# Performance work log

Measured on AMD Instinct MI355X. Metric: run time of the kernel, lower is better.

The kernel has to match this reference:

```python
import jax, jax.numpy as jnp
import numpy as np

N_NODES = 50000
LN_EPS = 1e-5


def gcn_conv(x, src, dst, norm, W, b):
    # PyG GCNConv: h = x @ W, then symmetric-normalized scatter-add, then bias.
    h = x @ W                                   # [N, out]
    msg = h[src] * norm[:, None]                # [E+N, out] gathered, scaled
    out = jax.ops.segment_sum(msg, dst, num_segments=N_NODES)
    return out + b


def layer_norm(x, gamma, beta):
    mu = jnp.mean(x, axis=-1, keepdims=True)
    var = jnp.var(x, axis=-1, keepdims=True)
    return (x - mu) * jax.lax.rsqrt(var + LN_EPS) * gamma + beta


def setup_inputs() -> dict:
    key = jax.random.key(0)
    ks = jax.random.split(key, 8)
    N, E, D = N_NODES, 1600000, 128
    x = jax.random.normal(ks[0], (N, D), dtype=jnp.float32)
    edge_index = jax.random.randint(ks[1], (2, E), 0, N, dtype=jnp.int64)
    s = 1.0 / np.sqrt(D)
    return {
        "x": x,
        "edge_index": edge_index,
        "W1": jax.random.uniform(ks[2], (D, D), jnp.float32, -s, s),
        "b1": jnp.zeros((D,), jnp.float32),
        "g1": jnp.ones((D,), jnp.float32),
        "be1": jnp.zeros((D,), jnp.float32),
        "W2": jax.random.uniform(ks[3], (D, D), jnp.float32, -s, s),
        "b2": jnp.zeros((D,), jnp.float32),
        "g2": jnp.ones((D,), jnp.float32),
        "be2": jnp.zeros((D,), jnp.float32),
    }


def reference(x, edge_index, W1, b1, g1, be1, W2, b2, g2, be2):
    # Add self-loops (PyG GCNConv default add_self_loops=True)
    sl = jnp.arange(N_NODES, dtype=edge_index.dtype)
    src = jnp.concatenate([edge_index[0], sl])
    dst = jnp.concatenate([edge_index[1], sl])
    # Symmetric normalization: deg^{-1/2}[src] * deg^{-1/2}[dst]
    deg = jax.ops.segment_sum(jnp.ones_like(src, dtype=x.dtype), dst,
                              num_segments=N_NODES)
    dinv = jnp.where(deg > 0, jax.lax.rsqrt(deg), 0.0)
    norm = dinv[src] * dinv[dst]

    h = gcn_conv(x, src, dst, norm, W1, b1)
    h = jax.nn.elu(layer_norm(h, g1, be1))
    h = gcn_conv(h, src, dst, norm, W2, b2)
    h = jax.nn.elu(layer_norm(h, g2, be2))
    return h
```

## Files before the change

### kernel.cpp

```cpp
#include <hip/hip_runtime.h>
#include <hip/hip_bf16.h>
#include <math.h>

#define N_NODES 50000
#define D 128
#define LN_EPS 1e-5f
#define NB 391
#define CHUNK 4096
#define GB 782
#define HB 512

typedef unsigned int u32;
typedef unsigned short u16;
typedef __attribute__((ext_vector_type(8))) short bf16x8;
typedef __attribute__((ext_vector_type(4))) float f32x4;

static __device__ __forceinline__ u16 f2bf(float f) {
    union { float f; unsigned u; } v; v.f = f;
    unsigned r = v.u + 0x7fff + ((v.u >> 16) & 1);
    return (u16)(r >> 16);
}
static __device__ __forceinline__ float bf2f(u16 b) {
    union { unsigned u; float f; } v; v.u = ((unsigned)b) << 16;
    return v.f;
}

static __device__ __forceinline__ bf16x8 packf8(const float* p) {
    float4 f0 = *(const float4*)p;
    float4 f1 = *(const float4*)(p + 4);
    bf16x8 r;
    r[0] = (short)f2bf(f0.x); r[1] = (short)f2bf(f0.y);
    r[2] = (short)f2bf(f0.z); r[3] = (short)f2bf(f0.w);
    r[4] = (short)f2bf(f1.x); r[5] = (short)f2bf(f1.y);
    r[6] = (short)f2bf(f1.z); r[7] = (short)f2bf(f1.w);
    return r;
}

__global__ __launch_bounds__(256) void gemm1_hist(const float* __restrict__ X,
                                                  const float* __restrict__ W,
                                                  u16* __restrict__ H,
                                                  const int* __restrict__ dstA,
                                                  u32* __restrict__ bucketCount, int E) {
    __shared__ __align__(16) u16 WT[D][136];
    __shared__ u32 hist[NB];

    if (blockIdx.x >= GB) {
        for (int b = threadIdx.x; b < NB; b += 256) hist[b] = 0;
        __syncthreads();
        int stride = HB * 256;
        for (int e = (blockIdx.x - GB) * 256 + threadIdx.x; e < E; e += stride)
            atomicAdd(&hist[((u32)dstA[e]) >> 7], 1u);
        __syncthreads();
        for (int b = threadIdx.x; b < NB; b += 256)
            if (hist[b]) atomicAdd(&bucketCount[b], hist[b]);
        return;
    }
    for (int idx = threadIdx.x; idx < D * D; idx += 256) {
        int k = idx >> 7, c = idx & 127;
        WT[c][k] = f2bf(W[idx]);
    }
    __syncthreads();

    int lane = threadIdx.x & 63;
    int wid  = threadIdx.x >> 6;
    int r    = lane & 15;
    int kg   = lane >> 4;

    for (int rb = blockIdx.x * 4 + wid; rb < N_NODES / 16; rb += GB * 4) {
        int row0 = rb * 16;
        const float* xp = X + (size_t)(row0 + r) * D + kg * 8;
        bf16x8 a0 = packf8(xp);      bf16x8 a1 = packf8(xp + 32);
        bf16x8 a2 = packf8(xp + 64); bf16x8 a3 = packf8(xp + 96);
#pragma unroll
        for (int tile = 0; tile < 8; ++tile) {
            const u16* wp = &WT[tile * 16 + r][kg * 8];
            f32x4 acc = {0.f, 0.f, 0.f, 0.f};
            acc = __builtin_amdgcn_mfma_f32_16x16x32_bf16(a0, *(const bf16x8*)(wp),      acc, 0, 0, 0);
            acc = __builtin_amdgcn_mfma_f32_16x16x32_bf16(a1, *(const bf16x8*)(wp + 32), acc, 0, 0, 0);
            acc = __builtin_amdgcn_mfma_f32_16x16x32_bf16(a2, *(const bf16x8*)(wp + 64), acc, 0, 0, 0);
            acc = __builtin_amdgcn_mfma_f32_16x16x32_bf16(a3, *(const bf16x8*)(wp + 96), acc, 0, 0, 0);
#pragma unroll
            for (int i = 0; i < 4; ++i)
                H[(size_t)(row0 + kg * 4 + i) * D + tile * 16 + r] = f2bf(acc[i]);
        }
    }
}

__global__ __launch_bounds__(256) void gemm_mfma(const u16* __restrict__ Xb,
                                                 const float* __restrict__ W,
                                                 u16* __restrict__ H) {
    __shared__ __align__(16) u16 WT[D][136];
    for (int idx = threadIdx.x; idx < D * D; idx += 256) {
        int k = idx >> 7, c = idx & 127;
        WT[c][k] = f2bf(W[idx]);
    }
    __syncthreads();
    int lane = threadIdx.x & 63;
    int wid  = threadIdx.x >> 6;
    int r    = lane & 15;
    int kg   = lane >> 4;
    for (int rb = blockIdx.x * 4 + wid; rb < N_NODES / 16; rb += GB * 4) {
        int row0 = rb * 16;
        const u16* xp = Xb + (size_t)(row0 + r) * D + kg * 8;
        bf16x8 a0 = *(const bf16x8*)(xp);      bf16x8 a1 = *(const bf16x8*)(xp + 32);
        bf16x8 a2 = *(const bf16x8*)(xp + 64); bf16x8 a3 = *(const bf16x8*)(xp + 96);
#pragma unroll
        for (int tile = 0; tile < 8; ++tile) {
            const u16* wp = &WT[tile * 16 + r][kg * 8];
            f32x4 acc = {0.f, 0.f, 0.f, 0.f};
            acc = __builtin_amdgcn_mfma_f32_16x16x32_bf16(a0, *(const bf16x8*)(wp),      acc, 0, 0, 0);
            acc = __builtin_amdgcn_mfma_f32_16x16x32_bf16(a1, *(const bf16x8*)(wp + 32), acc, 0, 0, 0);
            acc = __builtin_amdgcn_mfma_f32_16x16x32_bf16(a2, *(const bf16x8*)(wp + 64), acc, 0, 0, 0);
            acc = __builtin_amdgcn_mfma_f32_16x16x32_bf16(a3, *(const bf16x8*)(wp + 96), acc, 0, 0, 0);
#pragma unroll
            for (int i = 0; i < 4; ++i)
                H[(size_t)(row0 + kg * 4 + i) * D + tile * 16 + r] = f2bf(acc[i]);
        }
    }
}

__global__ __launch_bounds__(512) void partition_kernel(const int* __restrict__ srcA,
                                                        const int* __restrict__ dstA,
                                                        const u32* __restrict__ bucketCount,
                                                        u32* __restrict__ relCursor,
                                                        u32* __restrict__ ebuf, int E) {
    __shared__ u32 sc[512];
    __shared__ u32 ebS[NB], cntA[NB], cntB[NB], base[NB];
    int t = threadIdx.x;
    u32 bc = (t < NB) ? bucketCount[t] : 0u;
    sc[t] = bc;
    for (int b = t; b < NB; b += 512) { cntA[b] = 0; cntB[b] = 0; }
    __syncthreads();
    for (int off = 1; off < 512; off <<= 1) {
        u32 v = sc[t] + ((t >= off) ? sc[t - off] : 0u);
        __syncthreads();
        sc[t] = v;
        __syncthreads();
    }
    if (t < NB) ebS[t] = sc[t] - bc;
    __syncthreads();

    int e0 = blockIdx.x * CHUNK;
    int e1 = min(e0 + CHUNK, E);
    for (int e = e0 + t; e < e1; e += 512)
        atomicAdd(&cntA[((u32)dstA[e]) >> 7], 1u);
    __syncthreads();
    for (int b = t; b < NB; b += 512)
        if (cntA[b]) base[b] = ebS[b] + atomicAdd(&relCursor[b], cntA[b]);
    __syncthreads();
    for (int e = e0 + t; e < e1; e += 512) {
        u32 d = (u32)dstA[e], sv = (u32)srcA[e];
        u32 b = d >> 7;
        u32 off = atomicAdd(&cntB[b], 1u);
        ebuf[base[b] + off] = (sv << 16) | d;
    }
}

__global__ __launch_bounds__(256) void bucket_build(const u32* __restrict__ ebuf,
                                                    const u32* __restrict__ bucketCount,
                                                    u16* __restrict__ csr_src,
                                                    int* __restrict__ startArr,
                                                    int* __restrict__ deg,
                                                    float* __restrict__ dinv) {
    int b = blockIdx.x, t = threadIdx.x;
    __shared__ u32 red[256];
    __shared__ u32 cnt[128], sc[128], cur[128];
    u32 partial = 0;
    for (int i = t; i < b; i += 256) partial += bucketCount[i];
    red[t] = partial;
    if (t < 128) cnt[t] = 0;
    __syncthreads();
    for (int off = 128; off > 0; off >>= 1) {
        if (t < off) red[t] += red[t + off];
        __syncthreads();
    }
    u32 eb0 = red[0];
    u32 eb1 = eb0 + bucketCount[b];
    u32 cs  = eb0 + 128u * (u32)b;

    int nodeBase = b << 7;
    int nNodes = min(128, N_NODES - nodeBase);
    for (u32 e = eb0 + t; e < eb1; e += 256)
        atomicAdd(&cnt[ebuf[e] & 127u], 1u);
    __syncthreads();
    if (t < 128) sc[t] = (t < nNodes) ? cnt[t] + 1u : 0u;
    __syncthreads();
    for (int off = 1; off < 128; off <<= 1) {
        u32 v = 0;
        if (t < 128) v = sc[t] + ((t >= off) ? sc[t - off] : 0u);
        __syncthreads();
        if (t < 128) sc[t] = v;
        __syncthreads();
    }
    if (t < nNodes) {
        u32 val = cnt[t] + 1u;
        u32 excl = sc[t] - val;
        int i = nodeBase + t;
        deg[i] = (int)val;
        dinv[i] = rsqrtf((float)val);
        u32 sa = cs + excl;
        startArr[i] = (int)sa;
        csr_src[sa] = (u16)i;
        cur[t] = excl + 1u;
    }
    __syncthreads();
    for (u32 e = eb0 + t; e < eb1; e += 256) {
        u32 p = ebuf[e];
        u32 pos = atomicAdd(&cur[p & 127u], 1u);
        csr_src[cs + pos] = (u16)(p >> 16);
    }
}

template <int WRITE_BF16>
__global__ __launch_bounds__(256) void agg_ln_elu(
        const u16* __restrict__ H, const u16* __restrict__ csr_src,
        const int* __restrict__ startArr, const int* __restrict__ deg,
        const float* __restrict__ dinv,
        const float* __restrict__ bias, const float* __restrict__ gamma,
        const float* __restrict__ beta, void* __restrict__ outv) {
    int lane = threadIdx.x & 63;
    int wid  = threadIdx.x >> 6;
    int half = lane >> 5;
    int l    = lane & 31;
    int node = blockIdx.x * 8 + wid * 2 + half;

    int s    = startArr[node];
    int cnt  = deg[node];
    float dn = dinv[node];
    int c0   = l * 4;

    float a0 = 0.f, a1 = 0.f, a2 = 0.f, a3 = 0.f;
    float b0 = 0.f, b1 = 0.f, b2 = 0.f, b3 = 0.f;
    int j = 0;
    for (; j + 8 <= cnt; j += 8) {
        u32 i0 = csr_src[s + j],     i1 = csr_src[s + j + 1];
        u32 i2 = csr_src[s + j + 2], i3 = csr_src[s + j + 3];
        u32 i4 = csr_src[s + j + 4], i5 = csr_src[s + j + 5];
        u32 i6 = csr_src[s + j + 6], i7 = csr_src[s + j + 7];
        float w0 = dinv[i0] * dn, w1 = dinv[i1] * dn;
        float w2 = dinv[i2] * dn, w3 = dinv[i3] * dn;
        float w4 = dinv[i4] * dn, w5 = dinv[i5] * dn;
        float w6 = dinv[i6] * dn, w7 = dinv[i7] * dn;
        ushort4 g0 = *(const ushort4*)&H[(size_t)i0 * D + c0];
        ushort4 g1 = *(const ushort4*)&H[(size_t)i1 * D + c0];
        ushort4 g2 = *(const ushort4*)&H[(size_t)i2 * D + c0];
        ushort4 g3 = *(const ushort4*)&H[(size_t)i3 * D + c0];
        ushort4 g4 = *(const ushort4*)&H[(size_t)i4 * D + c0];
        ushort4 g5 = *(const ushort4*)&H[(size_t)i5 * D + c0];
        ushort4 g6 = *(const ushort4*)&H[(size_t)i6 * D + c0];
        ushort4 g7 = *(const ushort4*)&H[(size_t)i7 * D + c0];
        a0 = fmaf(w0, bf2f(g0.x), a0); a1 = fmaf(w0, bf2f(g0.y), a1);
        a2 = fmaf(w0, bf2f(g0.z), a2); a3 = fmaf(w0, bf2f(g0.w), a3);
        b0 = fmaf(w1, bf2f(g1.x), b0); b1 = fmaf(w1, bf2f(g1.y), b1);
        b2 = fmaf(w1, bf2f(g1.z), b2); b3 = fmaf(w1, bf2f(g1.w), b3);
        a0 = fmaf(w2, bf2f(g2.x), a0); a1 = fmaf(w2, bf2f(g2.y), a1);
        a2 = fmaf(w2, bf2f(g2.z), a2); a3 = fmaf(w2, bf2f(g2.w), a3);
        b0 = fmaf(w3, bf2f(g3.x), b0); b1 = fmaf(w3, bf2f(g3.y), b1);
        b2 = fmaf(w3, bf2f(g3.z), b2); b3 = fmaf(w3, bf2f(g3.w), b3);
        a0 = fmaf(w4, bf2f(g4.x), a0); a1 = fmaf(w4, bf2f(g4.y), a1);
        a2 = fmaf(w4, bf2f(g4.z), a2); a3 = fmaf(w4, bf2f(g4.w), a3);
        b0 = fmaf(w5, bf2f(g5.x), b0); b1 = fmaf(w5, bf2f(g5.y), b1);
        b2 = fmaf(w5, bf2f(g5.z), b2); b3 = fmaf(w5, bf2f(g5.w), b3);
        a0 = fmaf(w6, bf2f(g6.x), a0); a1 = fmaf(w6, bf2f(g6.y), a1);
        a2 = fmaf(w6, bf2f(g6.z), a2); a3 = fmaf(w6, bf2f(g6.w), a3);
        b0 = fmaf(w7, bf2f(g7.x), b0); b1 = fmaf(w7, bf2f(g7.y), b1);
        b2 = fmaf(w7, bf2f(g7.z), b2); b3 = fmaf(w7, bf2f(g7.w), b3);
    }
    for (; j < cnt; ++j) {
        u32 i0 = csr_src[s + j];
        float w0 = dinv[i0] * dn;
        ushort4 g0 = *(const ushort4*)&H[(size_t)i0 * D + c0];
        a0 = fmaf(w0, bf2f(g0.x), a0); a1 = fmaf(w0, bf2f(g0.y), a1);
        a2 = fmaf(w0, bf2f(g0.z), a2); a3 = fmaf(w0, bf2f(g0.w), a3);
    }
    a0 += b0; a1 += b1; a2 += b2; a3 += b3;

    float4 bv = *(const float4*)&bias[c0];
    a0 += bv.x; a1 += bv.y; a2 += bv.z; a3 += bv.w;

    float sum = a0 + a1 + a2 + a3;
    float sq  = a0 * a0 + a1 * a1 + a2 * a2 + a3 * a3;
#pragma unroll
    for (int m = 16; m > 0; m >>= 1) {
        sum += __shfl_xor(sum, m, 64);
        sq  += __shfl_xor(sq,  m, 64);
    }
    float mean = sum * (1.f / 128.f);
    float var  = sq * (1.f / 128.f) - mean * mean;
    float rstd = rsqrtf(var + LN_EPS);

    float4 gv = *(const float4*)&gamma[c0];
    float4 ev = *(const float4*)&beta[c0];
    float y0 = (a0 - mean) * rstd * gv.x + ev.x;
    float y1 = (a1 - mean) * rstd * gv.y + ev.y;
    float y2 = (a2 - mean) * rstd * gv.z + ev.z;
    float y3 = (a3 - mean) * rstd * gv.w + ev.w;
    y0 = y0 > 0.f ? y0 : expm1f(y0);
    y1 = y1 > 0.f ? y1 : expm1f(y1);
    y2 = y2 > 0.f ? y2 : expm1f(y2);
    y3 = y3 > 0.f ? y3 : expm1f(y3);

    if (WRITE_BF16) {
        ushort4 o;
        o.x = f2bf(y0); o.y = f2bf(y1); o.z = f2bf(y2); o.w = f2bf(y3);
        *(ushort4*)((u16*)outv + (size_t)node * D + c0) = o;
    } else {
        f32x4 o = {y0, y1, y2, y3};
        __builtin_nontemporal_store(o, (f32x4*)((float*)outv + (size_t)node * D + c0));
    }
}

extern "C" void kernel_launch(void* const* d_in, const int* in_sizes, int n_in,
                              void* d_out, int out_size, void* d_ws, size_t ws_size,
                              hipStream_t stream) {
    const float* x   = (const float*)d_in[0];
    const int*  eidx = (const int*)d_in[1];
    const float* W1  = (const float*)d_in[2];
    const float* b1  = (const float*)d_in[3];
    const float* g1  = (const float*)d_in[4];
    const float* be1 = (const float*)d_in[5];
    const float* W2  = (const float*)d_in[6];
    const float* b2  = (const float*)d_in[7];
    const float* g2  = (const float*)d_in[8];
    const float* be2 = (const float*)d_in[9];

    int E = in_sizes[1] / 2;
    const int* srcA = eidx;
    const int* dstA = eidx + E;

    char* p = (char*)d_ws;
    auto alloc = [&](size_t bytes) {
        char* r = p;
        p += (bytes + 255) & ~(size_t)255;
        return r;
    };
    u32*   ctr      = (u32*)alloc((size_t)1024 * 4);
    u32*   ebuf     = (u32*)alloc((size_t)E * 4);
    u16*   csr_src  = (u16*)alloc((size_t)(E + N_NODES) * 2);
    int*   startArr = (int*)alloc((size_t)N_NODES * 4);
    int*   deg      = (int*)alloc((size_t)N_NODES * 4);
    float* dinv     = (float*)alloc((size_t)N_NODES * 4);
    u16*   h        = (u16*)alloc((size_t)N_NODES * D * 2);
    u16*   x2b      = (u16*)alloc((size_t)N_NODES * D * 2);
    float* outp     = (float*)d_out;

    u32* bucketCount = ctr;
    u32* relCursor   = ctr + 512;

    int pb = (E + CHUNK - 1) / CHUNK;
    int ab = N_NODES / 8;

    hipMemsetAsync(ctr, 0, 1024 * 4, stream);
    gemm1_hist      <<<GB + HB, 256, 0, stream>>>(x, W1, h, dstA, bucketCount, E);
    partition_kernel<<<pb, 512, 0, stream>>>(srcA, dstA, bucketCount, relCursor, ebuf, E);
    bucket_build    <<<NB, 256, 0, stream>>>(ebuf, bucketCount, csr_src, startArr, deg, dinv);
    agg_ln_elu<1>   <<<ab, 256, 0, stream>>>(h, csr_src, startArr, deg, dinv,
                                             b1, g1, be1, x2b);
    gemm_mfma       <<<GB, 256, 0, stream>>>(x2b, W2, h);
    agg_ln_elu<0>   <<<ab, 256, 0, stream>>>(h, csr_src, startArr, deg, dinv,
                                             b2, g2, be2, outp);
}
```

Before: 285.6 us.

## Fuse layer-1 aggregation with layer-2 GEMM and precompute per-edge weights in CSR

Per-node degree is now counted with global atomics inside the partition kernel. The CSR stores (src, normalized weight) pairs, so aggregation no longer gathers dinv per edge. The first aggregate+LN+ELU is fused with the second GEMM in a new kernel that stages 16 rows in shared memory and runs MFMA, which removes the intermediate bf16 round trip and one launch. In exchange the CSR doubles in size to 8 bytes per edge, 1.6M global atomics are added for degree, and every fused block reloads and transposes W2 into LDS.

```diff
diff --git a/kernel.cpp b/kernel.cpp
--- a/kernel.cpp
+++ b/kernel.cpp
@@ -24,7 +24,6 @@
     union { unsigned u; float f; } v; v.u = ((unsigned)b) << 16;
     return v.f;
 }
-
 static __device__ __forceinline__ bf16x8 packf8(const float* p) {
     float4 f0 = *(const float4*)p;
     float4 f1 = *(const float4*)(p + 4);
@@ -34,6 +33,84 @@
     r[4] = (short)f2bf(f1.x); r[5] = (short)f2bf(f1.y);
     r[6] = (short)f2bf(f1.z); r[7] = (short)f2bf(f1.w);
     return r;
+}
+
+static __device__ __forceinline__ void agg_core(
+        const u16* __restrict__ H, const int2* __restrict__ csr,
+        int s, int cnt, int c0,
+        float& a0, float& a1, float& a2, float& a3) {
+    float b0 = 0.f, b1 = 0.f, b2 = 0.f, b3 = 0.f;
+    a0 = a1 = a2 = a3 = 0.f;
+    const int2* ce = csr + s;
+    int j = 0;
+    for (; j + 8 <= cnt; j += 8) {
+        int2 e0 = ce[j],     e1 = ce[j + 1], e2 = ce[j + 2], e3 = ce[j + 3];
+        int2 e4 = ce[j + 4], e5 = ce[j + 5], e6 = ce[j + 6], e7 = ce[j + 7];
+        ushort4 g0 = *(const ushort4*)&H[(size_t)(u32)e0.x * D + c0];
+        ushort4 g1 = *(const ushort4*)&H[(size_t)(u32)e1.x * D + c0];
+        ushort4 g2 = *(const ushort4*)&H[(size_t)(u32)e2.x * D + c0];
+        ushort4 g3 = *(const ushort4*)&H[(size_t)(u32)e3.x * D + c0];
+        ushort4 g4 = *(const ushort4*)&H[(size_t)(u32)e4.x * D + c0];
+        ushort4 g5 = *(const ushort4*)&H[(size_t)(u32)e5.x * D + c0];
+        ushort4 g6 = *(const ushort4*)&H[(size_t)(u32)e6.x * D + c0];
+        ushort4 g7 = *(const ushort4*)&H[(size_t)(u32)e7.x * D + c0];
+        float w0 = __int_as_float(e0.y), w1 = __int_as_float(e1.y);
+        float w2 = __int_as_float(e2.y), w3 = __int_as_float(e3.y);
+        float w4 = __int_as_float(e4.y), w5 = __int_as_float(e5.y);
+        float w6 = __int_as_float(e6.y), w7 = __int_as_float(e7.y);
+        a0 = fmaf(w0, bf2f(g0.x), a0); a1 = fmaf(w0, bf2f(g0.y), a1);
+        a2 = fmaf(w0, bf2f(g0.z), a2); a3 = fmaf(w0, bf2f(g0.w), a3);
+        b0 = fmaf(w1, bf2f(g1.x), b0); b1 = fmaf(w1, bf2f(g1.y), b1);
+        b2 = fmaf(w1, bf2f(g1.z), b2); b3 = fmaf(w1, bf2f(g1.w), b3);
+        a0 = fmaf(w2, bf2f(g2.x), a0); a1 = fmaf(w2, bf2f(g2.y), a1);
+        a2 = fmaf(w2, bf2f(g2.z), a2); a3 = fmaf(w2, bf2f(g2.w), a3);
+        b0 = fmaf(w3, bf2f(g3.x), b0); b1 = fmaf(w3, bf2f(g3.y), b1);
+        b2 = fmaf(w3, bf2f(g3.z), b2); b3 = fmaf(w3, bf2f(g3.w), b3);
+        a0 = fmaf(w4, bf2f(g4.x), a0); a1 = fmaf(w4, bf2f(g4.y), a1);
+        a2 = fmaf(w4, bf2f(g4.z), a2); a3 = fmaf(w4, bf2f(g4.w), a3);
+        b0 = fmaf(w5, bf2f(g5.x), b0); b1 = fmaf(w5, bf2f(g5.y), b1);
+        b2 = fmaf(w5, bf2f(g5.z), b2); b3 = fmaf(w5, bf2f(g5.w), b3);
+        a0 = fmaf(w6, bf2f(g6.x), a0); a1 = fmaf(w6, bf2f(g6.y), a1);
+        a2 = fmaf(w6, bf2f(g6.z), a2); a3 = fmaf(w6, bf2f(g6.w), a3);
+        b0 = fmaf(w7, bf2f(g7.x), b0); b1 = fmaf(w7, bf2f(g7.y), b1);
+        b2 = fmaf(w7, bf2f(g7.z), b2); b3 = fmaf(w7, bf2f(g7.w), b3);
+    }
+    for (; j < cnt; ++j) {
+        int2 e0 = ce[j];
+        ushort4 g0 = *(const ushort4*)&H[(size_t)(u32)e0.x * D + c0];
+        float w0 = __int_as_float(e0.y);
+        a0 = fmaf(w0, bf2f(g0.x), a0); a1 = fmaf(w0, bf2f(g0.y), a1);
+        a2 = fmaf(w0, bf2f(g0.z), a2); a3 = fmaf(w0, bf2f(g0.w), a3);
+    }
+    a0 += b0; a1 += b1; a2 += b2; a3 += b3;
+}
+
+static __device__ __forceinline__ void ln_elu(
+        float& a0, float& a1, float& a2, float& a3, int c0,
+        const float* __restrict__ bias, const float* __restrict__ gamma,
+        const float* __restrict__ beta) {
+    float4 bv = *(const float4*)&bias[c0];
+    a0 += bv.x; a1 += bv.y; a2 += bv.z; a3 += bv.w;
+    float sum = a0 + a1 + a2 + a3;
+    float sq  = a0 * a0 + a1 * a1 + a2 * a2 + a3 * a3;
+#pragma unroll
+    for (int m = 16; m > 0; m >>= 1) {
+        sum += __shfl_xor(sum, m, 64);
+        sq  += __shfl_xor(sq,  m, 64);
+    }
+    float mean = sum * (1.f / 128.f);
+    float var  = sq * (1.f / 128.f) - mean * mean;
+    float rstd = rsqrtf(var + LN_EPS);
+    float4 gv = *(const float4*)&gamma[c0];
+    float4 ev = *(const float4*)&beta[c0];
+    a0 = (a0 - mean) * rstd * gv.x + ev.x;
+    a1 = (a1 - mean) * rstd * gv.y + ev.y;
+    a2 = (a2 - mean) * rstd * gv.z + ev.z;
+    a3 = (a3 - mean) * rstd * gv.w + ev.w;
+    a0 = a0 > 0.f ? a0 : expm1f(a0);
+    a1 = a1 > 0.f ? a1 : expm1f(a1);
+    a2 = a2 > 0.f ? a2 : expm1f(a2);
+    a3 = a3 > 0.f ? a3 : expm1f(a3);
 }
 
 __global__ __launch_bounds__(256) void gemm1_hist(const float* __restrict__ X,
@@ -86,43 +163,11 @@
     }
 }
 
-__global__ __launch_bounds__(256) void gemm_mfma(const u16* __restrict__ Xb,
-                                                 const float* __restrict__ W,
-                                                 u16* __restrict__ H) {
-    __shared__ __align__(16) u16 WT[D][136];
-    for (int idx = threadIdx.x; idx < D * D; idx += 256) {
-        int k = idx >> 7, c = idx & 127;
-        WT[c][k] = f2bf(W[idx]);
-    }
-    __syncthreads();
-    int lane = threadIdx.x & 63;
-    int wid  = threadIdx.x >> 6;
-    int r    = lane & 15;
-    int kg   = lane >> 4;
-    for (int rb = blockIdx.x * 4 + wid; rb < N_NODES / 16; rb += GB * 4) {
-        int row0 = rb * 16;
-        const u16* xp = Xb + (size_t)(row0 + r) * D + kg * 8;
-        bf16x8 a0 = *(const bf16x8*)(xp);      bf16x8 a1 = *(const bf16x8*)(xp + 32);
-        bf16x8 a2 = *(const bf16x8*)(xp + 64); bf16x8 a3 = *(const bf16x8*)(xp + 96);
-#pragma unroll
-        for (int tile = 0; tile < 8; ++tile) {
-            const u16* wp = &WT[tile * 16 + r][kg * 8];
-            f32x4 acc = {0.f, 0.f, 0.f, 0.f};
-            acc = __builtin_amdgcn_mfma_f32_16x16x32_bf16(a0, *(const bf16x8*)(wp),      acc, 0, 0, 0);
-            acc = __builtin_amdgcn_mfma_f32_16x16x32_bf16(a1, *(const bf16x8*)(wp + 32), acc, 0, 0, 0);
-            acc = __builtin_amdgcn_mfma_f32_16x16x32_bf16(a2, *(const bf16x8*)(wp + 64), acc, 0, 0, 0);
-            acc = __builtin_amdgcn_mfma_f32_16x16x32_bf16(a3, *(const bf16x8*)(wp + 96), acc, 0, 0, 0);
-#pragma unroll
-            for (int i = 0; i < 4; ++i)
-                H[(size_t)(row0 + kg * 4 + i) * D + tile * 16 + r] = f2bf(acc[i]);
-        }
-    }
-}
-
 __global__ __launch_bounds__(512) void partition_kernel(const int* __restrict__ srcA,
                                                         const int* __restrict__ dstA,
                                                         const u32* __restrict__ bucketCount,
                                                         u32* __restrict__ relCursor,
+                                                        u32* __restrict__ deg,
                                                         u32* __restrict__ ebuf, int E) {
     __shared__ u32 sc[512];
     __shared__ u32 ebS[NB], cntA[NB], cntB[NB], base[NB];
@@ -142,8 +187,11 @@
 
     int e0 = blockIdx.x * CHUNK;
     int e1 = min(e0 + CHUNK, E);
-    for (int e = e0 + t; e < e1; e += 512)
-        atomicAdd(&cntA[((u32)dstA[e]) >> 7], 1u);
+    for (int e = e0 + t; e < e1; e += 512) {
+        u32 d = (u32)dstA[e];
+        atomicAdd(&cntA[d >> 7], 1u);
+        atomicAdd(&deg[d], 1u);
+    }
     __syncthreads();
     for (int b = t; b < NB; b += 512)
         if (cntA[b]) base[b] = ebS[b] + atomicAdd(&relCursor[b], cntA[b]);
@@ -158,17 +206,16 @@
 
 __global__ __launch_bounds__(256) void bucket_build(const u32* __restrict__ ebuf,
                                                     const u32* __restrict__ bucketCount,
-                                                    u16* __restrict__ csr_src,
-                                                    int* __restrict__ startArr,
-                                                    int* __restrict__ deg,
-                                                    float* __restrict__ dinv) {
+                                                    const u32* __restrict__ deg,
+                                                    int2* __restrict__ csr,
+                                                    int* __restrict__ startArr) {
     int b = blockIdx.x, t = threadIdx.x;
     __shared__ u32 red[256];
-    __shared__ u32 cnt[128], sc[128], cur[128];
+    __shared__ u32 sc[128], cur[128];
+    __shared__ float dloc[128];
     u32 partial = 0;
     for (int i = t; i < b; i += 256) partial += bucketCount[i];
     red[t] = partial;
-    if (t < 128) cnt[t] = 0;
     __syncthreads();
     for (int off = 128; off > 0; off >>= 1) {
         if (t < off) red[t] += red[t + off];
@@ -180,10 +227,12 @@
 
     int nodeBase = b << 7;
     int nNodes = min(128, N_NODES - nodeBase);
-    for (u32 e = eb0 + t; e < eb1; e += 256)
-        atomicAdd(&cnt[ebuf[e] & 127u], 1u);
-    __syncthreads();
-    if (t < 128) sc[t] = (t < nNodes) ? cnt[t] + 1u : 0u;
+    u32 myCnt = 0;
+    if (t < 128) {
+        myCnt = (t < nNodes) ? deg[nodeBase + t] + 1u : 0u;
+        sc[t] = myCnt;
+        dloc[t] = (t < nNodes) ? rsqrtf((float)myCnt) : 0.f;
+    }
     __syncthreads();
     for (int off = 1; off < 128; off <<= 1) {
         u32 v = 0;
@@ -193,121 +242,99 @@
         __syncthreads();
     }
     if (t < nNodes) {
-        u32 val = cnt[t] + 1u;
-        u32 excl = sc[t] - val;
+        u32 excl = sc[t] - myCnt;
         int i = nodeBase + t;
-        deg[i] = (int)val;
-        dinv[i] = rsqrtf((float)val);
-        u32 sa = cs + excl;
-        startArr[i] = (int)sa;
-        csr_src[sa] = (u16)i;
+        startArr[i] = (int)(cs + excl);
+        float di = dloc[t];
+        int2 v; v.x = i; v.y = __float_as_int(di * di);
+        csr[cs + excl] = v;
         cur[t] = excl + 1u;
+        if (b == NB - 1 && t == nNodes - 1)
+            startArr[N_NODES] = (int)(cs + sc[t]);
     }
     __syncthreads();
     for (u32 e = eb0 + t; e < eb1; e += 256) {
         u32 p = ebuf[e];
-        u32 pos = atomicAdd(&cur[p & 127u], 1u);
-        csr_src[cs + pos] = (u16)(p >> 16);
-    }
-}
-
-template <int WRITE_BF16>
+        u32 node = p & 127u;
+        u32 src  = p >> 16;
+        u32 pos = atomicAdd(&cur[node], 1u);
+        float w = dloc[node] * rsqrtf((float)(deg[src] + 1u));
+        int2 v; v.x = (int)src; v.y = __float_as_int(w);
+        csr[cs + pos] = v;
+    }
+}
+
+__global__ __launch_bounds__(512) void agg_gemm(
+        const u16* __restrict__ H, const int2* __restrict__ csr,
+        const int* __restrict__ startArr,
+        const float* __restrict__ bias, const float* __restrict__ gamma,
+        const float* __restrict__ beta,
+        const float* __restrict__ W2, u16* __restrict__ H2) {
+    __shared__ __align__(16) u16 WT[D][136];
+    __shared__ __align__(16) u16 X2[16][136];
+
+    int t = threadIdx.x;
+    for (int idx = t; idx < D * D; idx += 512) {
+        int k = idx >> 7, c = idx & 127;
+        WT[c][k] = f2bf(W2[idx]);
+    }
+
+    int xr  = t >> 5;
+    int l   = t & 31;
+    int c0  = l * 4;
+    int node = blockIdx.x * 16 + xr;
+    int s   = startArr[node];
+    int cnt = startArr[node + 1] - s;
+
+    float a0, a1, a2, a3;
+    agg_core(H, csr, s, cnt, c0, a0, a1, a2, a3);
+    ln_elu(a0, a1, a2, a3, c0, bias, gamma, beta);
+
+    ushort4 o;
+    o.x = f2bf(a0); o.y = f2bf(a1); o.z = f2bf(a2); o.w = f2bf(a3);
+    *(ushort4*)&X2[xr][c0] = o;
+    __syncthreads();
+
+    int lane = t & 63;
+    int w    = t >> 6;
+    int r    = lane & 15;
+    int kg   = lane >> 4;
+    int row0 = blockIdx.x * 16;
+
+    const u16* xp = &X2[r][kg * 8];
+    bf16x8 a0f = *(const bf16x8*)(xp);
+    bf16x8 a1f = *(const bf16x8*)(xp + 32);
+    bf16x8 a2f = *(const bf16x8*)(xp + 64);
+    bf16x8 a3f = *(const bf16x8*)(xp + 96);
+    const u16* wp = &WT[w * 16 + r][kg * 8];
+    f32x4 acc = {0.f, 0.f, 0.f, 0.f};
+    acc = __builtin_amdgcn_mfma_f32_16x16x32_bf16(a0f, *(const bf16x8*)(wp),      acc, 0, 0, 0);
+    acc = __builtin_amdgcn_mfma_f32_16x16x32_bf16(a1f, *(const bf16x8*)(wp + 32), acc, 0, 0, 0);
+    acc = __builtin_amdgcn_mfma_f32_16x16x32_bf16(a2f, *(const bf16x8*)(wp + 64), acc, 0, 0, 0);
+    acc = __builtin_amdgcn_mfma_f32_16x16x32_bf16(a3f, *(const bf16x8*)(wp + 96), acc, 0, 0, 0);
+#pragma unroll
+    for (int i = 0; i < 4; ++i)
+        H2[(size_t)(row0 + kg * 4 + i) * D + w * 16 + r] = f2bf(acc[i]);
+}
+
 __global__ __launch_bounds__(256) void agg_ln_elu(
-        const u16* __restrict__ H, const u16* __restrict__ csr_src,
-        const int* __restrict__ startArr, const int* __restrict__ deg,
-        const float* __restrict__ dinv,
+        const u16* __restrict__ H, const int2* __restrict__ csr,
+        const int* __restrict__ startArr,
         const float* __restrict__ bias, const float* __restrict__ gamma,
-        const float* __restrict__ beta, void* __restrict__ outv) {
-    int lane = threadIdx.x & 63;
-    int wid  = threadIdx.x >> 6;
-    int half = lane >> 5;
-    int l    = lane & 31;
-    int node = blockIdx.x * 8 + wid * 2 + half;
-
+        const float* __restrict__ beta, float* __restrict__ out) {
+    int t = threadIdx.x;
+    int node = blockIdx.x * 8 + (t >> 5);
+    int l    = t & 31;
+    int c0   = l * 4;
     int s    = startArr[node];
-    int cnt  = deg[node];
-    float dn = dinv[node];
-    int c0   = l * 4;
-
-    float a0 = 0.f, a1 = 0.f, a2 = 0.f, a3 = 0.f;
-    float b0 = 0.f, b1 = 0.f, b2 = 0.f, b3 = 0.f;
-    int j = 0;
-    for (; j + 8 <= cnt; j += 8) {
-        u32 i0 = csr_src[s + j],     i1 = csr_src[s + j + 1];
-        u32 i2 = csr_src[s + j + 2], i3 = csr_src[s + j + 3];
-        u32 i4 = csr_src[s + j + 4], i5 = csr_src[s + j + 5];
-        u32 i6 = csr_src[s + j + 6], i7 = csr_src[s + j + 7];
-        float w0 = dinv[i0] * dn, w1 = dinv[i1] * dn;
-        float w2 = dinv[i2] * dn, w3 = dinv[i3] * dn;
-        float w4 = dinv[i4] * dn, w5 = dinv[i5] * dn;
-        float w6 = dinv[i6] * dn, w7 = dinv[i7] * dn;
-        ushort4 g0 = *(const ushort4*)&H[(size_t)i0 * D + c0];
-        ushort4 g1 = *(const ushort4*)&H[(size_t)i1 * D + c0];
-        ushort4 g2 = *(const ushort4*)&H[(size_t)i2 * D + c0];
-        ushort4 g3 = *(const ushort4*)&H[(size_t)i3 * D + c0];
-        ushort4 g4 = *(const ushort4*)&H[(size_t)i4 * D + c0];
-        ushort4 g5 = *(const ushort4*)&H[(size_t)i5 * D + c0];
-        ushort4 g6 = *(const ushort4*)&H[(size_t)i6 * D + c0];
-        ushort4 g7 = *(const ushort4*)&H[(size_t)i7 * D + c0];
-        a0 = fmaf(w0, bf2f(g0.x), a0); a1 = fmaf(w0, bf2f(g0.y), a1);
-        a2 = fmaf(w0, bf2f(g0.z), a2); a3 = fmaf(w0, bf2f(g0.w), a3);
-        b0 = fmaf(w1, bf2f(g1.x), b0); b1 = fmaf(w1, bf2f(g1.y), b1);
-        b2 = fmaf(w1, bf2f(g1.z), b2); b3 = fmaf(w1, bf2f(g1.w), b3);
-        a0 = fmaf(w2, bf2f(g2.x), a0); a1 = fmaf(w2, bf2f(g2.y), a1);
-        a2 = fmaf(w2, bf2f(g2.z), a2); a3 = fmaf(w2, bf2f(g2.w), a3);
-        b0 = fmaf(w3, bf2f(g3.x), b0); b1 = fmaf(w3, bf2f(g3.y), b1);
-        b2 = fmaf(w3, bf2f(g3.z), b2); b3 = fmaf(w3, bf2f(g3.w), b3);
-        a0 = fmaf(w4, bf2f(g4.x), a0); a1 = fmaf(w4, bf2f(g4.y), a1);
-        a2 = fmaf(w4, bf2f(g4.z), a2); a3 = fmaf(w4, bf2f(g4.w), a3);
-        b0 = fmaf(w5, bf2f(g5.x), b0); b1 = fmaf(w5, bf2f(g5.y), b1);
-        b2 = fmaf(w5, bf2f(g5.z), b2); b3 = fmaf(w5, bf2f(g5.w), b3);
-        a0 = fmaf(w6, bf2f(g6.x), a0); a1 = fmaf(w6, bf2f(g6.y), a1);
-        a2 = fmaf(w6, bf2f(g6.z), a2); a3 = fmaf(w6, bf2f(g6.w), a3);
-        b0 = fmaf(w7, bf2f(g7.x), b0); b1 = fmaf(w7, bf2f(g7.y), b1);
-        b2 = fmaf(w7, bf2f(g7.z), b2); b3 = fmaf(w7, bf2f(g7.w), b3);
-    }
-    for (; j < cnt; ++j) {
-        u32 i0 = csr_src[s + j];
-        float w0 = dinv[i0] * dn;
-        ushort4 g0 = *(const ushort4*)&H[(size_t)i0 * D + c0];
-        a0 = fmaf(w0, bf2f(g0.x), a0); a1 = fmaf(w0, bf2f(g0.y), a1);
-        a2 = fmaf(w0, bf2f(g0.z), a2); a3 = fmaf(w0, bf2f(g0.w), a3);
-    }
-    a0 += b0; a1 += b1; a2 += b2; a3 += b3;
-
-    float4 bv = *(const float4*)&bias[c0];
-    a0 += bv.x; a1 += bv.y; a2 += bv.z; a3 += bv.w;
-
-    float sum = a0 + a1 + a2 + a3;
-    float sq  = a0 * a0 + a1 * a1 + a2 * a2 + a3 * a3;
-#pragma unroll
-    for (int m = 16; m > 0; m >>= 1) {
-        sum += __shfl_xor(sum, m, 64);
-        sq  += __shfl_xor(sq,  m, 64);
-    }
-    float mean = sum * (1.f / 128.f);
-    float var  = sq * (1.f / 128.f) - mean * mean;
-    float rstd = rsqrtf(var + LN_EPS);
-
-    float4 gv = *(const float4*)&gamma[c0];
-    float4 ev = *(const float4*)&beta[c0];
-    float y0 = (a0 - mean) * rstd * gv.x + ev.x;
-    float y1 = (a1 - mean) * rstd * gv.y + ev.y;
-    float y2 = (a2 - mean) * rstd * gv.z + ev.z;
-    float y3 = (a3 - mean) * rstd * gv.w + ev.w;
-    y0 = y0 > 0.f ? y0 : expm1f(y0);
-    y1 = y1 > 0.f ? y1 : expm1f(y1);
-    y2 = y2 > 0.f ? y2 : expm1f(y2);
-    y3 = y3 > 0.f ? y3 : expm1f(y3);
-
-    if (WRITE_BF16) {
-        ushort4 o;
-        o.x = f2bf(y0); o.y = f2bf(y1); o.z = f2bf(y2); o.w = f2bf(y3);
-        *(ushort4*)((u16*)outv + (size_t)node * D + c0) = o;
-    } else {
-        f32x4 o = {y0, y1, y2, y3};
-        __builtin_nontemporal_store(o, (f32x4*)((float*)outv + (size_t)node * D + c0));
-    }
+    int cnt  = startArr[node + 1] - s;
+
+    float a0, a1, a2, a3;
+    agg_core(H, csr, s, cnt, c0, a0, a1, a2, a3);
+    ln_elu(a0, a1, a2, a3, c0, bias, gamma, beta);
+
+    f32x4 o = {a0, a1, a2, a3};
+    __builtin_nontemporal_store(o, (f32x4*)(out + (size_t)node * D + c0));
 }
 
 extern "C" void kernel_launch(void* const* d_in, const int* in_sizes, int n_in,
@@ -334,29 +361,27 @@
         p += (bytes + 255) & ~(size_t)255;
         return r;
     };
-    u32*   ctr      = (u32*)alloc((size_t)1024 * 4);
-    u32*   ebuf     = (u32*)alloc((size_t)E * 4);
-    u16*   csr_src  = (u16*)alloc((size_t)(E + N_NODES) * 2);
-    int*   startArr = (int*)alloc((size_t)N_NODES * 4);
-    int*   deg      = (int*)alloc((size_t)N_NODES * 4);
-    float* dinv     = (float*)alloc((size_t)N_NODES * 4);
-    u16*   h        = (u16*)alloc((size_t)N_NODES * D * 2);
-    u16*   x2b      = (u16*)alloc((size_t)N_NODES * D * 2);
-    float* outp     = (float*)d_out;
-
-    u32* bucketCount = ctr;
-    u32* relCursor   = ctr + 512;
+    u32*   zeroRegion = (u32*)alloc((size_t)(1024 + N_NODES) * 4);
+    u32*   ebuf       = (u32*)alloc((size_t)E * 4);
+    int2*  csr        = (int2*)alloc((size_t)(E + N_NODES) * 8);
+    int*   startArr   = (int*)alloc((size_t)(N_NODES + 1) * 4);
+    u16*   h          = (u16*)alloc((size_t)N_NODES * D * 2);
+    u16*   h2         = (u16*)alloc((size_t)N_NODES * D * 2);
+    float* outp       = (float*)d_out;
+
+    u32* bucketCount = zeroRegion;
+    u32* relCursor   = zeroRegion + 512;
+    u32* deg         = zeroRegion + 1024;
 
     int pb = (E + CHUNK - 1) / CHUNK;
+    int fb = N_NODES / 16;
     int ab = N_NODES / 8;
 
-    hipMemsetAsync(ctr, 0, 1024 * 4, stream);
+    hipError_t e0 = hipMemsetAsync(zeroRegion, 0, (size_t)(1024 + N_NODES) * 4, stream);
+    (void)e0;
     gemm1_hist      <<<GB + HB, 256, 0, stream>>>(x, W1, h, dstA, bucketCount, E);
-    partition_kernel<<<pb, 512, 0, stream>>>(srcA, dstA, bucketCount, relCursor, ebuf, E);
-    bucket_build    <<<NB, 256, 0, stream>>>(ebuf, bucketCount, csr_src, startArr, deg, dinv);
-    agg_ln_elu<1>   <<<ab, 256, 0, stream>>>(h, csr_src, startArr, deg, dinv,
-                                             b1, g1, be1, x2b);
-    gemm_mfma       <<<GB, 256, 0, stream>>>(x2b, W2, h);
-    agg_ln_elu<0>   <<<ab, 256, 0, stream>>>(h, csr_src, startArr, deg, dinv,
-                                             b2, g2, be2, outp);
-}
+    partition_kernel<<<pb, 512, 0, stream>>>(srcA, dstA, bucketCount, relCursor, deg, ebuf, E);
+    bucket_build    <<<NB, 256, 0, stream>>>(ebuf, bucketCount, deg, csr, startArr);
+    agg_gemm        <<<fb, 512, 0, stream>>>(h, csr, startArr, b1, g1, be1, W2, h2);
+    agg_ln_elu      <<<ab, 256, 0, stream>>>(h2, csr, startArr, b2, g2, be2, outp);
+}
```

After: 328.2 us. 1.15x slower.

## Fuse layer-1 aggregation/LayerNorm/ELU with second GEMM; widen per-lane gather to 8 columns

Applied to the files above, without the earlier changes.

Merges the first aggregation+LN+ELU kernel with the second MFMA GEMM, so the 16 normalized rows of each block are staged in shared memory and multiplied by W2 directly, skipping the bf16 intermediate round trip through global memory and one launch. Aggregation now uses 16 lanes per node with 16-byte gathers of 8 bf16 columns. The deg array is replaced by a startArr of N+1 entries, with degree taken from consecutive offsets. In exchange every aggregation block rebuilds the full transposed W2 tile in shared memory (3125 blocks doing 16K converts each), which adds load traffic and LDS pressure that may lower occupancy.

```diff
diff --git a/kernel.cpp b/kernel.cpp
--- a/kernel.cpp
+++ b/kernel.cpp
@@ -13,6 +13,7 @@
 typedef unsigned int u32;
 typedef unsigned short u16;
 typedef __attribute__((ext_vector_type(8))) short bf16x8;
+typedef __attribute__((ext_vector_type(8))) unsigned short u16x8;
 typedef __attribute__((ext_vector_type(4))) float f32x4;
 
 static __device__ __forceinline__ u16 f2bf(float f) {
@@ -24,7 +25,6 @@
     union { unsigned u; float f; } v; v.u = ((unsigned)b) << 16;
     return v.f;
 }
-
 static __device__ __forceinline__ bf16x8 packf8(const float* p) {
     float4 f0 = *(const float4*)p;
     float4 f1 = *(const float4*)(p + 4);
@@ -36,6 +36,85 @@
     return r;
 }
 
+static __device__ __forceinline__ void agg_core8(
+        const u16* __restrict__ H, const u16* __restrict__ csr_src,
+        const float* __restrict__ dinv, int s, int cnt, int c0, float dn,
+        float* __restrict__ a) {
+    float b[8];
+#pragma unroll
+    for (int i = 0; i < 8; ++i) { a[i] = 0.f; b[i] = 0.f; }
+    const u16* cp = csr_src + s;
+    int j = 0;
+    for (; j + 8 <= cnt; j += 8) {
+        u32 i0 = cp[j],     i1 = cp[j + 1], i2 = cp[j + 2], i3 = cp[j + 3];
+        u32 i4 = cp[j + 4], i5 = cp[j + 5], i6 = cp[j + 6], i7 = cp[j + 7];
+        u16x8 g0 = *(const u16x8*)&H[(size_t)i0 * D + c0];
+        u16x8 g1 = *(const u16x8*)&H[(size_t)i1 * D + c0];
+        u16x8 g2 = *(const u16x8*)&H[(size_t)i2 * D + c0];
+        u16x8 g3 = *(const u16x8*)&H[(size_t)i3 * D + c0];
+        u16x8 g4 = *(const u16x8*)&H[(size_t)i4 * D + c0];
+        u16x8 g5 = *(const u16x8*)&H[(size_t)i5 * D + c0];
+        u16x8 g6 = *(const u16x8*)&H[(size_t)i6 * D + c0];
+        u16x8 g7 = *(const u16x8*)&H[(size_t)i7 * D + c0];
+        float w0 = dinv[i0] * dn, w1 = dinv[i1] * dn;
+        float w2 = dinv[i2] * dn, w3 = dinv[i3] * dn;
+        float w4 = dinv[i4] * dn, w5 = dinv[i5] * dn;
+        float w6 = dinv[i6] * dn, w7 = dinv[i7] * dn;
+#pragma unroll
+        for (int i = 0; i < 8; ++i) {
+            a[i] = fmaf(w0, bf2f(g0[i]), a[i]);
+            b[i] = fmaf(w1, bf2f(g1[i]), b[i]);
+            a[i] = fmaf(w2, bf2f(g2[i]), a[i]);
+            b[i] = fmaf(w3, bf2f(g3[i]), b[i]);
+            a[i] = fmaf(w4, bf2f(g4[i]), a[i]);
+            b[i] = fmaf(w5, bf2f(g5[i]), b[i]);
+            a[i] = fmaf(w6, bf2f(g6[i]), a[i]);
+            b[i] = fmaf(w7, bf2f(g7[i]), b[i]);
+        }
+    }
+    for (; j < cnt; ++j) {
+        u32 i0 = cp[j];
+        u16x8 g0 = *(const u16x8*)&H[(size_t)i0 * D + c0];
+        float w0 = dinv[i0] * dn;
+#pragma unroll
+        for (int i = 0; i < 8; ++i) a[i] = fmaf(w0, bf2f(g0[i]), a[i]);
+    }
+#pragma unroll
+    for (int i = 0; i < 8; ++i) a[i] += b[i];
+}
+
+static __device__ __forceinline__ void ln_elu8(
+        float* __restrict__ a, int c0,
+        const float* __restrict__ bias, const float* __restrict__ gamma,
+        const float* __restrict__ beta) {
+    float4 bv0 = *(const float4*)&bias[c0];
+    float4 bv1 = *(const float4*)&bias[c0 + 4];
+    a[0] += bv0.x; a[1] += bv0.y; a[2] += bv0.z; a[3] += bv0.w;
+    a[4] += bv1.x; a[5] += bv1.y; a[6] += bv1.z; a[7] += bv1.w;
+    float sum = 0.f, sq = 0.f;
+#pragma unroll
+    for (int i = 0; i < 8; ++i) { sum += a[i]; sq = fmaf(a[i], a[i], sq); }
+#pragma unroll
+    for (int m = 8; m > 0; m >>= 1) {
+        sum += __shfl_xor(sum, m, 64);
+        sq  += __shfl_xor(sq,  m, 64);
+    }
+    float mean = sum * (1.f / 128.f);
+    float var  = sq * (1.f / 128.f) - mean * mean;
+    float rstd = rsqrtf(var + LN_EPS);
+    float4 gv0 = *(const float4*)&gamma[c0];
+    float4 gv1 = *(const float4*)&gamma[c0 + 4];
+    float4 ev0 = *(const float4*)&beta[c0];
+    float4 ev1 = *(const float4*)&beta[c0 + 4];
+    float gg[8] = {gv0.x, gv0.y, gv0.z, gv0.w, gv1.x, gv1.y, gv1.z, gv1.w};
+    float ee[8] = {ev0.x, ev0.y, ev0.z, ev0.w, ev1.x, ev1.y, ev1.z, ev1.w};
+#pragma unroll
+    for (int i = 0; i < 8; ++i) {
+        float y = (a[i] - mean) * rstd * gg[i] + ee[i];
+        a[i] = y > 0.f ? y : expm1f(y);
+    }
+}
+
 __global__ __launch_bounds__(256) void gemm1_hist(const float* __restrict__ X,
                                                   const float* __restrict__ W,
                                                   u16* __restrict__ H,
@@ -71,39 +150,6 @@
         const float* xp = X + (size_t)(row0 + r) * D + kg * 8;
         bf16x8 a0 = packf8(xp);      bf16x8 a1 = packf8(xp + 32);
         bf16x8 a2 = packf8(xp + 64); bf16x8 a3 = packf8(xp + 96);
-#pragma unroll
-        for (int tile = 0; tile < 8; ++tile) {
-            const u16* wp = &WT[tile * 16 + r][kg * 8];
-            f32x4 acc = {0.f, 0.f, 0.f, 0.f};
-            acc = __builtin_amdgcn_mfma_f32_16x16x32_bf16(a0, *(const bf16x8*)(wp),      acc, 0, 0, 0);
-            acc = __builtin_amdgcn_mfma_f32_16x16x32_bf16(a1, *(const bf16x8*)(wp + 32), acc, 0, 0, 0);
-            acc = __builtin_amdgcn_mfma_f32_16x16x32_bf16(a2, *(const bf16x8*)(wp + 64), acc, 0, 0, 0);
-            acc = __builtin_amdgcn_mfma_f32_16x16x32_bf16(a3, *(const bf16x8*)(wp + 96), acc, 0, 0, 0);
-#pragma unroll
-            for (int i = 0; i < 4; ++i)
-                H[(size_t)(row0 + kg * 4 + i) * D + tile * 16 + r] = f2bf(acc[i]);
-        }
-    }
-}
-
-__global__ __launch_bounds__(256) void gemm_mfma(const u16* __restrict__ Xb,
-                                                 const float* __restrict__ W,
-                                                 u16* __restrict__ H) {
-    __shared__ __align__(16) u16 WT[D][136];
-    for (int idx = threadIdx.x; idx < D * D; idx += 256) {
-        int k = idx >> 7, c = idx & 127;
-        WT[c][k] = f2bf(W[idx]);
-    }
-    __syncthreads();
-    int lane = threadIdx.x & 63;
-    int wid  = threadIdx.x >> 6;
-    int r    = lane & 15;
-    int kg   = lane >> 4;
-    for (int rb = blockIdx.x * 4 + wid; rb < N_NODES / 16; rb += GB * 4) {
-        int row0 = rb * 16;
-        const u16* xp = Xb + (size_t)(row0 + r) * D + kg * 8;
-        bf16x8 a0 = *(const bf16x8*)(xp);      bf16x8 a1 = *(const bf16x8*)(xp + 32);
-        bf16x8 a2 = *(const bf16x8*)(xp + 64); bf16x8 a3 = *(const bf16x8*)(xp + 96);
 #pragma unroll
         for (int tile = 0; tile < 8; ++tile) {
             const u16* wp = &WT[tile * 16 + r][kg * 8];
@@ -160,7 +206,6 @@
                                                     const u32* __restrict__ bucketCount,
                                                     u16* __restrict__ csr_src,
                                                     int* __restrict__ startArr,
-                                                    int* __restrict__ deg,
                                                     float* __restrict__ dinv) {
     int b = blockIdx.x, t = threadIdx.x;
     __shared__ u32 red[256];
@@ -183,7 +228,11 @@
     for (u32 e = eb0 + t; e < eb1; e += 256)
         atomicAdd(&cnt[ebuf[e] & 127u], 1u);
     __syncthreads();
-    if (t < 128) sc[t] = (t < nNodes) ? cnt[t] + 1u : 0u;
+    u32 myCnt = 0;
+    if (t < 128) {
+        myCnt = (t < nNodes) ? cnt[t] + 1u : 0u;
+        sc[t] = myCnt;
+    }
     __syncthreads();
     for (int off = 1; off < 128; off <<= 1) {
         u32 v = 0;
@@ -193,15 +242,14 @@
         __syncthreads();
     }
     if (t < nNodes) {
-        u32 val = cnt[t] + 1u;
-        u32 excl = sc[t] - val;
+        u32 excl = sc[t] - myCnt;
         int i = nodeBase + t;
-        deg[i] = (int)val;
-        dinv[i] = rsqrtf((float)val);
-        u32 sa = cs + excl;
-        startArr[i] = (int)sa;
-        csr_src[sa] = (u16)i;
+        startArr[i] = (int)(cs + excl);
+        dinv[i] = rsqrtf((float)myCnt);
+        csr_src[cs + excl] = (u16)i;
         cur[t] = excl + 1u;
+        if (b == NB - 1 && t == nNodes - 1)
+            startArr[N_NODES] = (int)(cs + sc[t]);
     }
     __syncthreads();
     for (u32 e = eb0 + t; e < eb1; e += 256) {
@@ -211,103 +259,86 @@
     }
 }
 
-template <int WRITE_BF16>
+__global__ __launch_bounds__(256) void agg_gemm(
+        const u16* __restrict__ H, const u16* __restrict__ csr_src,
+        const int* __restrict__ startArr, const float* __restrict__ dinv,
+        const float* __restrict__ bias, const float* __restrict__ gamma,
+        const float* __restrict__ beta,
+        const float* __restrict__ W2, u16* __restrict__ H2) {
+    __shared__ __align__(16) u16 WT[D][136];
+    __shared__ __align__(16) u16 X2[16][136];
+
+    int t = threadIdx.x;
+    for (int idx = t; idx < D * D; idx += 256) {
+        int k = idx >> 7, c = idx & 127;
+        WT[c][k] = f2bf(W2[idx]);
+    }
+
+    int grp = t >> 4;
+    int l   = t & 15;
+    int c0  = l * 8;
+    int node = blockIdx.x * 16 + grp;
+    int s   = startArr[node];
+    int cnt = startArr[node + 1] - s;
+    float dn = dinv[node];
+
+    float a[8];
+    agg_core8(H, csr_src, dinv, s, cnt, c0, dn, a);
+    ln_elu8(a, c0, bias, gamma, beta);
+
+    u16x8 o;
+#pragma unroll
+    for (int i = 0; i < 8; ++i) o[i] = f2bf(a[i]);
+    *(u16x8*)&X2[grp][c0] = o;
+    __syncthreads();
+
+    int lane = t & 63;
+    int wv   = t >> 6;
+    int r    = lane & 15;
+    int kg   = lane >> 4;
+    int row0 = blockIdx.x * 16;
+
+    const u16* xp = &X2[r][kg * 8];
+    bf16x8 a0f = *(const bf16x8*)(xp);
+    bf16x8 a1f = *(const bf16x8*)(xp + 32);
+    bf16x8 a2f = *(const bf16x8*)(xp + 64);
+    bf16x8 a3f = *(const bf16x8*)(xp + 96);
+#pragma unroll
+    for (int tile = wv; tile < 8; tile += 4) {
+        const u16* wp = &WT[tile * 16 + r][kg * 8];
+        f32x4 acc = {0.f, 0.f, 0.f, 0.f};
+        acc = __builtin_amdgcn_mfma_f32_16x16x32_bf16(a0f, *(const bf16x8*)(wp),      acc, 0, 0, 0);
+        acc = __builtin_amdgcn_mfma_f32_16x16x32_bf16(a1f, *(const bf16x8*)(wp + 32), acc, 0, 0, 0);
+        acc = __builtin_amdgcn_mfma_f32_16x16x32_bf16(a2f, *(const bf16x8*)(wp + 64), acc, 0, 0, 0);
+        acc = __builtin_amdgcn_mfma_f32_16x16x32_bf16(a3f, *(const bf16x8*)(wp + 96), acc, 0, 0, 0);
+#pragma unroll
+        for (int i = 0; i < 4; ++i)
+            H2[(size_t)(row0 + kg * 4 + i) * D + tile * 16 + r] = f2bf(acc[i]);
+    }
+}
+
 __global__ __launch_bounds__(256) void agg_ln_elu(
         const u16* __restrict__ H, const u16* __restrict__ csr_src,
-        const int* __restrict__ startArr, const int* __restrict__ deg,
-        const float* __restrict__ dinv,
+        const int* __restrict__ startArr, const float* __restrict__ dinv,
         const float* __restrict__ bias, const float* __restrict__ gamma,
-        const float* __restrict__ beta, void* __restrict__ outv) {
-    int lane = threadIdx.x & 63;
-    int wid  = threadIdx.x >> 6;
-    int half = lane >> 5;
-    int l    = lane & 31;
-    int node = blockIdx.x * 8 + wid * 2 + half;
-
+        const float* __restrict__ beta, float* __restrict__ out) {
+    int t = threadIdx.x;
+    int node = blockIdx.x * 16 + (t >> 4);
+    int l    = t & 15;
+    int c0   = l * 8;
     int s    = startArr[node];
-    int cnt  = deg[node];
+    int cnt  = startArr[node + 1] - s;
     float dn = dinv[node];
-    int c0   = l * 4;
-
-    float a0 = 0.f, a1 = 0.f, a2 = 0.f, a3 = 0.f;
-    float b0 = 0.f, b1 = 0.f, b2 = 0.f, b3 = 0.f;
-    int j = 0;
-    for (; j + 8 <= cnt; j += 8) {
-        u32 i0 = csr_src[s + j],     i1 = csr_src[s + j + 1];
-        u32 i2 = csr_src[s + j + 2], i3 = csr_src[s + j + 3];
-        u32 i4 = csr_src[s + j + 4], i5 = csr_src[s + j + 5];
-        u32 i6 = csr_src[s + j + 6], i7 = csr_src[s + j + 7];
-        float w0 = dinv[i0] * dn, w1 = dinv[i1] * dn;
-        float w2 = dinv[i2] * dn, w3 = dinv[i3] * dn;
-        float w4 = dinv[i4] * dn, w5 = dinv[i5] * dn;
-        float w6 = dinv[i6] * dn, w7 = dinv[i7] * dn;
-        ushort4 g0 = *(const ushort4*)&H[(size_t)i0 * D + c0];
-        ushort4 g1 = *(const ushort4*)&H[(size_t)i1 * D + c0];
-        ushort4 g2 = *(const ushort4*)&H[(size_t)i2 * D + c0];
-        ushort4 g3 = *(const ushort4*)&H[(size_t)i3 * D + c0];
-        ushort4 g4 = *(const ushort4*)&H[(size_t)i4 * D + c0];
-        ushort4 g5 = *(const ushort4*)&H[(size_t)i5 * D + c0];
-        ushort4 g6 = *(const ushort4*)&H[(size_t)i6 * D + c0];
-        ushort4 g7 = *(const ushort4*)&H[(size_t)i7 * D + c0];
-        a0 = fmaf(w0, bf2f(g0.x), a0); a1 = fmaf(w0, bf2f(g0.y), a1);
-        a2 = fmaf(w0, bf2f(g0.z), a2); a3 = fmaf(w0, bf2f(g0.w), a3);
-        b0 = fmaf(w1, bf2f(g1.x), b0); b1 = fmaf(w1, bf2f(g1.y), b1);
-        b2 = fmaf(w1, bf2f(g1.z), b2); b3 = fmaf(w1, bf2f(g1.w), b3);
-        a0 = fmaf(w2, bf2f(g2.x), a0); a1 = fmaf(w2, bf2f(g2.y), a1);
-        a2 = fmaf(w2, bf2f(g2.z), a2); a3 = fmaf(w2, bf2f(g2.w), a3);
-        b0 = fmaf(w3, bf2f(g3.x), b0); b1 = fmaf(w3, bf2f(g3.y), b1);
-        b2 = fmaf(w3, bf2f(g3.z), b2); b3 = fmaf(w3, bf2f(g3.w), b3);
-        a0 = fmaf(w4, bf2f(g4.x), a0); a1 = fmaf(w4, bf2f(g4.y), a1);
-        a2 = fmaf(w4, bf2f(g4.z), a2); a3 = fmaf(w4, bf2f(g4.w), a3);
-        b0 = fmaf(w5, bf2f(g5.x), b0); b1 = fmaf(w5, bf2f(g5.y), b1);
-        b2 = fmaf(w5, bf2f(g5.z), b2); b3 = fmaf(w5, bf2f(g5.w), b3);
-        a0 = fmaf(w6, bf2f(g6.x), a0); a1 = fmaf(w6, bf2f(g6.y), a1);
-        a2 = fmaf(w6, bf2f(g6.z), a2); a3 = fmaf(w6, bf2f(g6.w), a3);
-        b0 = fmaf(w7, bf2f(g7.x), b0); b1 = fmaf(w7, bf2f(g7.y), b1);
-        b2 = fmaf(w7, bf2f(g7.z), b2); b3 = fmaf(w7, bf2f(g7.w), b3);
-    }
-    for (; j < cnt; ++j) {
-        u32 i0 = csr_src[s + j];
-        float w0 = dinv[i0] * dn;
-        ushort4 g0 = *(const ushort4*)&H[(size_t)i0 * D + c0];
-        a0 = fmaf(w0, bf2f(g0.x), a0); a1 = fmaf(w0, bf2f(g0.y), a1);
-        a2 = fmaf(w0, bf2f(g0.z), a2); a3 = fmaf(w0, bf2f(g0.w), a3);
-    }
-    a0 += b0; a1 += b1; a2 += b2; a3 += b3;
-
-    float4 bv = *(const float4*)&bias[c0];
-    a0 += bv.x; a1 += bv.y; a2 += bv.z; a3 += bv.w;
-
-    float sum = a0 + a1 + a2 + a3;
-    float sq  = a0 * a0 + a1 * a1 + a2 * a2 + a3 * a3;
-#pragma unroll
-    for (int m = 16; m > 0; m >>= 1) {
-        sum += __shfl_xor(sum, m, 64);
-        sq  += __shfl_xor(sq,  m, 64);
-    }
-    float mean = sum * (1.f / 128.f);
-    float var  = sq * (1.f / 128.f) - mean * mean;
-    float rstd = rsqrtf(var + LN_EPS);
-
-    float4 gv = *(const float4*)&gamma[c0];
-    float4 ev = *(const float4*)&beta[c0];
-    float y0 = (a0 - mean) * rstd * gv.x + ev.x;
-    float y1 = (a1 - mean) * rstd * gv.y + ev.y;
-    float y2 = (a2 - mean) * rstd * gv.z + ev.z;
-    float y3 = (a3 - mean) * rstd * gv.w + ev.w;
-    y0 = y0 > 0.f ? y0 : expm1f(y0);
-    y1 = y1 > 0.f ? y1 : expm1f(y1);
-    y2 = y2 > 0.f ? y2 : expm1f(y2);
-    y3 = y3 > 0.f ? y3 : expm1f(y3);
-
-    if (WRITE_BF16) {
-        ushort4 o;
-        o.x = f2bf(y0); o.y = f2bf(y1); o.z = f2bf(y2); o.w = f2bf(y3);
-        *(ushort4*)((u16*)outv + (size_t)node * D + c0) = o;
-    } else {
-        f32x4 o = {y0, y1, y2, y3};
-        __builtin_nontemporal_store(o, (f32x4*)((float*)outv + (size_t)node * D + c0));
-    }
+
+    float a[8];
+    agg_core8(H, csr_src, dinv, s, cnt, c0, dn, a);
+    ln_elu8(a, c0, bias, gamma, beta);
+
+    f32x4 o0 = {a[0], a[1], a[2], a[3]};
+    f32x4 o1 = {a[4], a[5], a[6], a[7]};
+    float* op = out + (size_t)node * D + c0;
+    __builtin_nontemporal_store(o0, (f32x4*)op);
+    __builtin_nontemporal_store(o1, (f32x4*)(op + 4));
 }
 
 extern "C" void kernel_launch(void* const* d_in, const int* in_sizes, int n_in,
@@ -337,26 +368,25 @@
     u32*   ctr      = (u32*)alloc((size_t)1024 * 4);
     u32*   ebuf     = (u32*)alloc((size_t)E * 4);
     u16*   csr_src  = (u16*)alloc((size_t)(E + N_NODES) * 2);
-    int*   startArr = (int*)alloc((size_t)N_NODES * 4);
-    int*   deg      = (int*)alloc((size_t)N_NODES * 4);
+    int*   startArr = (int*)alloc((size_t)(N_NODES + 1) * 4);
     float* dinv     = (float*)alloc((size_t)N_NODES * 4);
     u16*   h        = (u16*)alloc((size_t)N_NODES * D * 2);
-    u16*   x2b      = (u16*)alloc((size_t)N_NODES * D * 2);
+    u16*   h2       = (u16*)alloc((size_t)N_NODES * D * 2);
     float* outp     = (float*)d_out;
 
     u32* bucketCount = ctr;
     u32* relCursor   = ctr + 512;
 
     int pb = (E + CHUNK - 1) / CHUNK;
-    int ab = N_NODES / 8;
-
-    hipMemsetAsync(ctr, 0, 1024 * 4, stream);
+    int fb = N_NODES / 16;
+
+    hipError_t e0 = hipMemsetAsync(ctr, 0, 1024 * 4, stream);
+    (void)e0;
     gemm1_hist      <<<GB + HB, 256, 0, stream>>>(x, W1, h, dstA, bucketCount, E);
     partition_kernel<<<pb, 512, 0, stream>>>(srcA, dstA, bucketCount, relCursor, ebuf, E);
-    bucket_build    <<<NB, 256, 0, stream>>>(ebuf, bucketCount, csr_src, startArr, deg, dinv);
-    agg_ln_elu<1>   <<<ab, 256, 0, stream>>>(h, csr_src, startArr, deg, dinv,
-                                             b1, g1, be1, x2b);
-    gemm_mfma       <<<GB, 256, 0, stream>>>(x2b, W2, h);
-    agg_ln_elu<0>   <<<ab, 256, 0, stream>>>(h, csr_src, startArr, deg, dinv,
+    bucket_build    <<<NB, 256, 0, stream>>>(ebuf, bucketCount, csr_src, startArr, dinv);
+    agg_gemm        <<<fb, 256, 0, stream>>>(h, csr_src, startArr, dinv,
+                                             b1, g1, be1, W2, h2);
+    agg_ln_elu      <<<fb, 256, 0, stream>>>(h2, csr_src, startArr, dinv,
                                              b2, g2, be2, outp);
 }
```

Measured after the change: 273.7 us. 4.2% less time.
